# Kernel optimization log

Measured on AMD Instinct MI355X. Metric: run time of the kernel, lower is better.

Reference implementation:

```python
import jax, jax.numpy as jnp
import numpy as np

EPS = 1e-5

def _conv(x, w, b):
    # NCHW x OIHW -> NCHW, stride 1, SAME padding (stencil center (1,1) of 3x3, or 1x1)
    y = jax.lax.conv_general_dilated(x, w, (1, 1), 'SAME',
                                     dimension_numbers=('NCHW', 'OIHW', 'NCHW'))
    return y + b[None, :, None, None]

def _bn(x, gamma, beta):
    # training-mode batchnorm: stats over (N, H, W) per channel
    mean = jnp.mean(x, axis=(0, 2, 3), keepdims=True)
    var = jnp.var(x, axis=(0, 2, 3), keepdims=True)
    xhat = (x - mean) * jax.lax.rsqrt(var + EPS)
    return xhat * gamma[None, :, None, None] + beta[None, :, None, None]

def setup_inputs() -> dict:
    key = jax.random.key(0)
    ks = jax.random.split(key, 12)
    B, Cin, Cout, H, W = 2, 64, 64, 512, 512
    s = 0.05
    return {
        'x':  jax.random.normal(ks[0], (B, Cin, H, W), jnp.float32),
        'w1': jax.random.normal(ks[1], (Cout, Cin, 3, 3), jnp.float32) * s,
        'b1': jnp.zeros((Cout,), jnp.float32),
        'g1': jnp.ones((Cout,), jnp.float32),
        'be1': jnp.zeros((Cout,), jnp.float32),
        'w2': jax.random.normal(ks[2], (Cout, Cout, 3, 3), jnp.float32) * s,
        'b2': jnp.zeros((Cout,), jnp.float32),
        'g2': jnp.ones((Cout,), jnp.float32),
        'be2': jnp.zeros((Cout,), jnp.float32),
        'wp': jax.random.normal(ks[3], (Cout, Cin, 1, 1), jnp.float32) * s,
        'bp': jnp.zeros((Cout,), jnp.float32),
        'gp': jnp.ones((Cout,), jnp.float32),
        'bep': jnp.zeros((Cout,), jnp.float32),
    }

def reference(x, w1, b1, g1, be1, w2, b2, g2, be2, wp, bp, gp, bep):
    # project branch: 1x1 conv ([(0,0)] stencil) + BN
    residual = _bn(_conv(x, wp, bp), gp, bep)
    # conv1: pad + 3x3 lattice conv (full cp stencil) + BN + Identity downsample + ReLU
    out = jax.nn.relu(_bn(_conv(x, w1, b1), g1, be1))
    # conv2: pad + 3x3 lattice conv + BN
    out = _bn(_conv(out, w2, b2), g2, be2)
    # residual add + output ReLU
    return jax.nn.relu(out + residual)
```

## Files before the change

kernel.cpp:

```cpp
#include <hip/hip_runtime.h>
#include <hip/hip_bf16.h>
#include <stdint.h>

typedef short short8 __attribute__((ext_vector_type(8)));
typedef float f32x4 __attribute__((ext_vector_type(4)));
typedef float f32x16 __attribute__((ext_vector_type(16)));
typedef unsigned int u32;
typedef unsigned short u16;

#define HH 512
#define WW 512
#define CC 64
#define PLANE (HH*WW)
#define NSTATF 524288.0f

#define KTW 32
#define HSTR1 560
#define KBSTR1 1120
#define SLOTB1 4480
#define RING1 (8*SLOTB1)
#define HSTR2 592
#define KBSTR2 1184
#define SLOTB2 4736
#define NSLOT2 10
#define RING2 (NSLOT2*SLOTB2)
#define BOUNCEB 16384
#define NBC1 1024
#define NBC2 2048
#define K5S 132

__device__ __forceinline__ u16 f2bf(float f) {
  __hip_bfloat16 h = __float2bfloat16(f);
  return __builtin_bit_cast(u16, h);
}
__device__ __forceinline__ u32 pk2bf(float a, float b) {
  return (u32)f2bf(a) | ((u32)f2bf(b) << 16);
}
__device__ __forceinline__ float bf2f(u16 u) {
  u32 x = ((u32)u) << 16;
  return __builtin_bit_cast(float, x);
}
__device__ __forceinline__ void lds_barrier() {
  asm volatile("s_waitcnt lgkmcnt(0)" ::: "memory");
  __builtin_amdgcn_s_barrier();
  __builtin_amdgcn_sched_barrier(0);
}

__global__ __launch_bounds__(512) void kprep(const float* __restrict__ w1,
    const float* __restrict__ w2, const float* __restrict__ wp,
    u16* __restrict__ wb1, u16* __restrict__ wb2, u16* __restrict__ wbp)
{
  const int id = blockIdx.x*512 + threadIdx.x;
  const int lane = id & 63;
  if (id < 4608) {
    const int fid = id >> 6;
    const int ct4 = fid / 18, rem = fid % 18;
    const int tap = rem >> 1, kb = rem & 1;
    const int cout = ct4*16 + (lane & 15);
    const int k0c = kb*32 + (lane >> 4)*8;
    u32 ow[4];
#pragma unroll
    for (int p = 0; p < 4; ++p) {
      ow[p] = pk2bf(w1[(size_t)(cout*64 + k0c + p*2)*9 + tap],
                    w1[(size_t)(cout*64 + k0c + p*2 + 1)*9 + tap]);
    }
    *(uint4*)(wb1 + ((size_t)fid*64 + lane)*8) = make_uint4(ow[0],ow[1],ow[2],ow[3]);
  } else if (id < 9216) {
    const int fid = (id - 4608) >> 6;
    const int ct = fid / 36, rem = fid % 36;
    const int tap = rem >> 2, kb = rem & 3;
    const int cout = ct*32 + (lane & 31);
    const int cinb = kb*16 + (lane >> 5)*8;
    u32 ow[4];
#pragma unroll
    for (int p = 0; p < 4; ++p) {
      ow[p] = pk2bf(w2[(size_t)(cout*64 + cinb + p*2)*9 + tap],
                    w2[(size_t)(cout*64 + cinb + p*2 + 1)*9 + tap]);
    }
    *(uint4*)(wb2 + ((size_t)fid*64 + lane)*8) = make_uint4(ow[0],ow[1],ow[2],ow[3]);
  } else if (id < 9728) {
    const int fid = (id - 9216) >> 6;
    const int ct4 = fid >> 1, kb = fid & 1;
    const int cout = ct4*16 + (lane & 15);
    const int k0c = kb*32 + (lane >> 4)*8;
    u32 ow[4];
#pragma unroll
    for (int p = 0; p < 4; ++p)
      ow[p] = pk2bf(wp[cout*64 + k0c + p*2], wp[cout*64 + k0c + p*2 + 1]);
    *(uint4*)(wbp + ((size_t)fid*64 + lane)*8) = make_uint4(ow[0],ow[1],ow[2],ow[3]);
  }
}

__global__ __launch_bounds__(256) void k0(const float* __restrict__ x, u16* __restrict__ xh)
{
  __shared__ __align__(16) u32 Tp[32*260];
  const int tid = threadIdx.x;
  const int wt = blockIdx.x, h = blockIdx.y, n = blockIdx.z;
  const int w0 = wt*256;
  const float* xp = x + (size_t)n*CC*PLANE + (size_t)h*WW + w0;
#pragma unroll
  for (int it = 0; it < 8; ++it) {
    const int j = it*256 + tid;
    const int c2 = j >> 6, w4 = (j & 63) << 2;
    const f32x4 a = *(const f32x4*)(xp + (size_t)(c2*2    )*PLANE + w4);
    const f32x4 b = *(const f32x4*)(xp + (size_t)(c2*2 + 1)*PLANE + w4);
    uint4 o;
    o.x = pk2bf(a[0], b[0]);
    o.y = pk2bf(a[1], b[1]);
    o.z = pk2bf(a[2], b[2]);
    o.w = pk2bf(a[3], b[3]);
    *(uint4*)(Tp + (u32)c2*260 + (u32)(w4 ^ (4*(c2 >> 2)))) = o;
  }
  __syncthreads();
  u16* op = xh + ((size_t)(n*HH + h)*WW + w0)*CC;
#pragma unroll
  for (int it = 0; it < 8; ++it) {
    const int j = it*256 + tid;
    const int w = j >> 3, c8 = j & 7;
    const u32 wsw = (u32)(w ^ (4*c8));
    uint4 o;
    o.x = Tp[(u32)(c8*4 + 0)*260 + wsw];
    o.y = Tp[(u32)(c8*4 + 1)*260 + wsw];
    o.z = Tp[(u32)(c8*4 + 2)*260 + wsw];
    o.w = Tp[(u32)(c8*4 + 3)*260 + wsw];
    *(uint4*)(op + (size_t)w*CC + c8*8) = o;
  }
}

__global__ __launch_bounds__(256, 2) void kconv1(const u16* __restrict__ in,
    const u16* __restrict__ wb, const u16* __restrict__ wbp,
    u16* __restrict__ out, u16* __restrict__ yp,
    float* __restrict__ ps, float* __restrict__ pq,
    float* __restrict__ psp, float* __restrict__ pqp)
{
  __shared__ __align__(16) char LB[RING1 + BOUNCEB + 512];
  const int tid = threadIdx.x;
  const int lane = tid & 63, wv = tid >> 6;
  const int l15 = lane & 15, lq = lane >> 4;
  const int wt = blockIdx.x, hs = blockIdx.y, n = blockIdx.z;
  const int w0 = wt*KTW, h0 = hs*16;
  const int bid = (n*32 + hs)*16 + wt;

  short8 wfr[18];
#pragma unroll
  for (int f = 0; f < 18; ++f)
    wfr[f] = *(const short8*)(wb + ((size_t)(wv*18 + f)*64 + lane)*8);
  short8 wpf[2];
#pragma unroll
  for (int kb = 0; kb < 2; ++kb)
    wpf[kb] = *(const short8*)(wbp + ((size_t)(wv*2 + kb)*64 + lane)*8);

  float s4[4] = {0,0,0,0}, q4[4] = {0,0,0,0};
  float sp4[4] = {0,0,0,0}, qp4[4] = {0,0,0,0};
  const u16* inb = in + (size_t)n*PLANE*CC;
  const u32 co0 = (u32)((lq >> 1)*KBSTR1 + (lq & 1)*HSTR1);
  const u32 co1 = co0 + 2*KBSTR1;

  auto ld_one = [&](int j, int cl, int c8) -> uint4 {
    const int gh = h0 - 1 + j, gw = w0 - 1 + cl;
    if (((u32)gh < (u32)HH) && ((u32)gw < (u32)WW))
      return *(const uint4*)(inb + ((size_t)gh*WW + gw)*CC + c8*8);
    return make_uint4(0u,0u,0u,0u);
  };
  auto st_one = [&](int slot, int cl, int c8, uint4 v) {
    *(uint4*)(LB + (size_t)slot*SLOTB1 + (c8>>1)*KBSTR1 + (c8&1)*HSTR1 + cl*16) = v;
  };

  for (int idx = tid; idx < 4*272; idx += 256) {
    const int jj = idx / 272, rem = idx - jj*272;
    st_one(jj, rem >> 3, rem & 7, ld_one(jj, rem >> 3, rem & 7));
  }
  __syncthreads();

  uint4 st0, st1, st2;
  auto issue2 = [&](int jb) {
    { const int idx = tid;       const int jj = idx/272, rem = idx - jj*272;
      st0 = ld_one(jb + jj, rem >> 3, rem & 7); }
    { const int idx = 256 + tid; const int jj = idx/272, rem = idx - jj*272;
      st1 = ld_one(jb + jj, rem >> 3, rem & 7); }
    if (tid < 32) { const int idx = 512 + tid; const int jj = idx/272, rem = idx - jj*272;
      st2 = ld_one(jb + jj, rem >> 3, rem & 7); }
  };
  auto write2 = [&](int jb) {
    { const int idx = tid;       const int jj = idx/272, rem = idx - jj*272;
      st_one((jb + jj) & 7, rem >> 3, rem & 7, st0); }
    { const int idx = 256 + tid; const int jj = idx/272, rem = idx - jj*272;
      st_one((jb + jj) & 7, rem >> 3, rem & 7, st1); }
    if (tid < 32) { const int idx = 512 + tid; const int jj = idx/272, rem = idx - jj*272;
      st_one((jb + jj) & 7, rem >> 3, rem & 7, st2); }
  };

  issue2(4);

  for (int g = 0; g < 8; ++g) {
    if (g > 0) write2(2*g + 2);
    lds_barrier();
    if (g < 7) issue2(2*g + 4);

    const char* sb[4];
#pragma unroll
    for (int mi = 0; mi < 4; ++mi)
      sb[mi] = LB + (size_t)((2*g + mi) & 7)*SLOTB1 + l15*16;
    f32x4 a0t0, a0t1, a1t0, a1t1;
    f32x4 p0t0, p0t1, p1t0, p1t1;
#pragma unroll
    for (int r = 0; r < 4; ++r) {
      a0t0[r]=0.f; a0t1[r]=0.f; a1t0[r]=0.f; a1t1[r]=0.f;
      p0t0[r]=0.f; p0t1[r]=0.f; p1t0[r]=0.f; p1t1[r]=0.f;
    }
#pragma unroll
    for (int t = 0; t < 2; ++t) {
      const int pb = t*16;
#pragma unroll
      for (int kb = 0; kb < 2; ++kb) {
        const u32 ck = kb ? co1 : co0;
#pragma unroll
        for (int mi = 0; mi < 4; ++mi) {
#pragma unroll
          for (int kw = 0; kw < 3; ++kw) {
            const short8 X = *(const short8*)(sb[mi] + ck + (u32)((pb + kw)*16));
            if (mi <= 2) {
              const short8 Wf = wfr[(mi*3 + kw)*2 + kb];
              if (t == 0) a0t0 = __builtin_amdgcn_mfma_f32_16x16x32_bf16(Wf, X, a0t0, 0,0,0);
              else        a0t1 = __builtin_amdgcn_mfma_f32_16x16x32_bf16(Wf, X, a0t1, 0,0,0);
            }
            if (mi >= 1) {
              const short8 Wf = wfr[((mi-1)*3 + kw)*2 + kb];
              if (t == 0) a1t0 = __builtin_amdgcn_mfma_f32_16x16x32_bf16(Wf, X, a1t0, 0,0,0);
              else        a1t1 = __builtin_amdgcn_mfma_f32_16x16x32_bf16(Wf, X, a1t1, 0,0,0);
            }
            if (kw == 1 && mi == 1) {
              if (t == 0) p0t0 = __builtin_amdgcn_mfma_f32_16x16x32_bf16(wpf[kb], X, p0t0, 0,0,0);
              else        p0t1 = __builtin_amdgcn_mfma_f32_16x16x32_bf16(wpf[kb], X, p0t1, 0,0,0);
            }
            if (kw == 1 && mi == 2) {
              if (t == 0) p1t0 = __builtin_amdgcn_mfma_f32_16x16x32_bf16(wpf[kb], X, p1t0, 0,0,0);
              else        p1t1 = __builtin_amdgcn_mfma_f32_16x16x32_bf16(wpf[kb], X, p1t1, 0,0,0);
            }
          }
        }
      }
    }
    {
      const int co = wv*16 + lq*4;
#pragma unroll
      for (int r = 0; r < 4; ++r) {
        s4[r] += a0t0[r] + a0t1[r] + a1t0[r] + a1t1[r];
        q4[r] = fmaf(a0t0[r], a0t0[r], q4[r]);
        q4[r] = fmaf(a0t1[r], a0t1[r], q4[r]);
        q4[r] = fmaf(a1t0[r], a1t0[r], q4[r]);
        q4[r] = fmaf(a1t1[r], a1t1[r], q4[r]);
        sp4[r] += p0t0[r] + p0t1[r] + p1t0[r] + p1t1[r];
        qp4[r] = fmaf(p0t0[r], p0t0[r], qp4[r]);
        qp4[r] = fmaf(p0t1[r], p0t1[r], qp4[r]);
        qp4[r] = fmaf(p1t0[r], p1t0[r], qp4[r]);
        qp4[r] = fmaf(p1t1[r], p1t1[r], qp4[r]);
      }
#pragma unroll
      for (int t = 0; t < 2; ++t) {
        const int pos = t*16 + l15;
        const u32 addr = ((u32)(pos*128 + co*2)) ^ (((u32)(pos & 7)) << 4);
        uint2 c0, c1, d0, d1;
        if (t == 0) {
          c0.x = pk2bf(a0t0[0], a0t0[1]); c0.y = pk2bf(a0t0[2], a0t0[3]);
          c1.x = pk2bf(a1t0[0], a1t0[1]); c1.y = pk2bf(a1t0[2], a1t0[3]);
          d0.x = pk2bf(p0t0[0], p0t0[1]); d0.y = pk2bf(p0t0[2], p0t0[3]);
          d1.x = pk2bf(p1t0[0], p1t0[1]); d1.y = pk2bf(p1t0[2], p1t0[3]);
        } else {
          c0.x = pk2bf(a0t1[0], a0t1[1]); c0.y = pk2bf(a0t1[2], a0t1[3]);
          c1.x = pk2bf(a1t1[0], a1t1[1]); c1.y = pk2bf(a1t1[2], a1t1[3]);
          d0.x = pk2bf(p0t1[0], p0t1[1]); d0.y = pk2bf(p0t1[2], p0t1[3]);
          d1.x = pk2bf(p1t1[0], p1t1[1]); d1.y = pk2bf(p1t1[2], p1t1[3]);
        }
        *(uint2*)(LB + RING1 + 0*4096 + addr) = c0;
        *(uint2*)(LB + RING1 + 1*4096 + addr) = c1;
        *(uint2*)(LB + RING1 + 2*4096 + addr) = d0;
        *(uint2*)(LB + RING1 + 3*4096 + addr) = d1;
      }
    }
    lds_barrier();
    {
      const int rowi = tid >> 6, tt = tid & 63;
      const int pos = tt >> 1, half = (tt & 1)*64;
      const char* bb = LB + RING1 + rowi*4096;
      u16* base = (rowi < 2) ? out : yp;
      const int orow = h0 + 2*g + (rowi & 1);
      char* dst = (char*)base + ((size_t)((n*HH + orow)*WW + w0 + pos))*128 + half;
      const u32 sw = ((u32)(pos & 7)) << 4;
#pragma unroll
      for (int k2 = 0; k2 < 4; ++k2) {
        const uint4 v = *(const uint4*)(bb + (((u32)(pos*128 + half + k2*16)) ^ sw));
        *(uint4*)(dst + k2*16) = v;
      }
    }
  }

#pragma unroll
  for (int d = 1; d <= 8; d <<= 1) {
#pragma unroll
    for (int r = 0; r < 4; ++r) {
      s4[r] += __shfl_xor(s4[r], d, 64);
      q4[r] += __shfl_xor(q4[r], d, 64);
      sp4[r] += __shfl_xor(sp4[r], d, 64);
      qp4[r] += __shfl_xor(qp4[r], d, 64);
    }
  }
  if (l15 == 0) {
#pragma unroll
    for (int r = 0; r < 4; ++r) {
      const int co = wv*16 + lq*4 + r;
      ps[(size_t)co*NBC1 + bid] = s4[r];
      pq[(size_t)co*NBC1 + bid] = q4[r];
      psp[(size_t)co*NBC1 + bid] = sp4[r];
      pqp[(size_t)co*NBC1 + bid] = qp4[r];
    }
  }
}

__global__ __launch_bounds__(256, 2) void kconv2(const u16* __restrict__ in,
    const u16* __restrict__ wb,
    const float* __restrict__ As, const float* __restrict__ Bs,
    u16* __restrict__ out, float* __restrict__ ps, float* __restrict__ pq)
{
  __shared__ __align__(16) char LB[RING2 + BOUNCEB + 512];
  float* sA = (float*)(LB + RING2 + BOUNCEB);
  float* sB = sA + 64;
  const int tid = threadIdx.x;
  const int lane = tid & 63, wv = tid >> 6;
  const int ct = wv & 1, ro = wv >> 1;
  const int wt = blockIdx.x, hs = blockIdx.y, n = blockIdx.z;
  const int w0 = wt*KTW, h0 = hs*16;
  const int bid = (n*32 + hs)*16 + wt;

  if (tid < 64) { sA[tid] = As[tid]; sB[tid] = Bs[tid]; }
  __syncthreads();

  short8 wfr[36];
#pragma unroll
  for (int f = 0; f < 36; ++f)
    wfr[f] = *(const short8*)(wb + ((size_t)(ct*36 + f)*64 + lane)*8);
  float s[16], q[16];
#pragma unroll
  for (int r = 0; r < 16; ++r) { s[r] = 0.f; q[r] = 0.f; }

  const u16* inb = in + (size_t)n*PLANE*CC;
  const u32 lt = (u32)((lane & 31)*16 + (lane >> 5)*HSTR2);

  auto ld_one = [&](int j, int cl, int c8) -> uint4 {
    const int gh = h0 - 1 + j, gw = w0 - 1 + cl;
    if (((u32)gh < (u32)HH) && ((u32)gw < (u32)WW))
      return *(const uint4*)(inb + ((size_t)gh*WW + gw)*CC + c8*8);
    return make_uint4(0u,0u,0u,0u);
  };
  auto st_one = [&](int slot, int cl, int c8, uint4 v) {
    const u32* uw = (const u32*)&v;
    u32 ow[4];
    const int cb = c8*8;
#pragma unroll
    for (int h2 = 0; h2 < 4; ++h2) {
      float f0 = fmaxf(bf2f((u16)(uw[h2] & 0xFFFFu)) * sA[cb+h2*2]   + sB[cb+h2*2],   0.f);
      float f1 = fmaxf(bf2f((u16)(uw[h2] >> 16))     * sA[cb+h2*2+1] + sB[cb+h2*2+1], 0.f);
      ow[h2] = pk2bf(f0, f1);
    }
    *(uint4*)(LB + (size_t)slot*SLOTB2 + (c8>>1)*KBSTR2 + (c8&1)*HSTR2 + cl*16) =
        make_uint4(ow[0],ow[1],ow[2],ow[3]);
  };

  for (int idx = tid; idx < 6*272; idx += 256) {
    const int jj = idx / 272, rem = idx - jj*272;
    st_one(jj, rem >> 3, rem & 7, ld_one(jj, rem >> 3, rem & 7));
  }
  __syncthreads();

  for (int g = 0; g < 4; ++g) {
    const bool dostage = (g <= 2);
    const int jb = 4*g + 6;
    uint4 st0, st1, st2, st3, st4;
    if (dostage) {
      { const int idx = tid;        const int jj = idx/272, rem = idx - jj*272;
        st0 = ld_one(jb + jj, rem >> 3, rem & 7); }
      { const int idx = 256 + tid;  const int jj = idx/272, rem = idx - jj*272;
        st1 = ld_one(jb + jj, rem >> 3, rem & 7); }
      { const int idx = 512 + tid;  const int jj = idx/272, rem = idx - jj*272;
        st2 = ld_one(jb + jj, rem >> 3, rem & 7); }
      { const int idx = 768 + tid;  const int jj = idx/272, rem = idx - jj*272;
        st3 = ld_one(jb + jj, rem >> 3, rem & 7); }
      if (tid < 64) { const int idx = 1024 + tid; const int jj = idx/272, rem = idx - jj*272;
        st4 = ld_one(jb + jj, rem >> 3, rem & 7); }
    }

    const int r0 = 4*g + 2*ro;
    f32x16 acc0, acc1;
#pragma unroll
    for (int rr = 0; rr < 16; ++rr) { acc0[rr] = 0.f; acc1[rr] = 0.f; }
    {
      const char* bm[4];
#pragma unroll
      for (int mi = 0; mi < 4; ++mi) {
        int sl = r0 + mi; if (sl >= NSLOT2) sl -= NSLOT2;
        bm[mi] = LB + (size_t)sl*SLOTB2 + lt;
      }
#pragma unroll
      for (int kb = 0; kb < 4; ++kb) {
#pragma unroll
        for (int mi = 0; mi < 4; ++mi) {
          const char* bp_ = bm[mi] + kb*KBSTR2;
#pragma unroll
          for (int kw = 0; kw < 3; ++kw) {
            const short8 X = *(const short8*)(bp_ + kw*16);
            if (mi <= 2)
              acc0 = __builtin_amdgcn_mfma_f32_32x32x16_bf16(wfr[(mi*3+kw)*4+kb], X, acc0, 0,0,0);
            if (mi >= 1)
              acc1 = __builtin_amdgcn_mfma_f32_32x32x16_bf16(wfr[((mi-1)*3+kw)*4+kb], X, acc1, 0,0,0);
          }
        }
      }
    }
    {
      const int pos = lane & 31;
      const int cob = ct*32 + 4*(lane>>5);
#pragma unroll
      for (int rr = 0; rr < 16; ++rr) {
        const float v0 = acc0[rr], v1 = acc1[rr];
        s[rr] += v0 + v1;
        q[rr] = fmaf(v0, v0, q[rr]);
        q[rr] = fmaf(v1, v1, q[rr]);
      }
#pragma unroll
      for (int k = 0; k < 4; ++k) {
        const u32 addr = ((u32)(pos*128 + (cob + 8*k)*2)) ^ (((u32)(pos & 7)) << 4);
        uint2 p0, p1;
        p0.x = pk2bf(acc0[4*k],   acc0[4*k+1]);
        p0.y = pk2bf(acc0[4*k+2], acc0[4*k+3]);
        p1.x = pk2bf(acc1[4*k],   acc1[4*k+1]);
        p1.y = pk2bf(acc1[4*k+2], acc1[4*k+3]);
        *(uint2*)(LB + RING2 + (2*ro    )*4096 + addr) = p0;
        *(uint2*)(LB + RING2 + (2*ro + 1)*4096 + addr) = p1;
      }
    }
    lds_barrier();
    {
      const int rowi = tid >> 6, tt = tid & 63;
      const int pos = tt >> 1, half = (tt & 1)*64;
      const char* bb = LB + RING2 + rowi*4096;
      char* dst = (char*)out + ((size_t)((n*HH + h0 + 4*g + rowi)*WW + w0 + pos))*128 + half;
      const u32 sw = ((u32)(pos & 7)) << 4;
#pragma unroll
      for (int k2 = 0; k2 < 4; ++k2) {
        const uint4 v = *(const uint4*)(bb + (((u32)(pos*128 + half + k2*16)) ^ sw));
        *(uint4*)(dst + k2*16) = v;
      }
    }
    if (dostage) {
      { const int idx = tid;        const int jj = idx/272, rem = idx - jj*272;
        int sl = jb + jj; if (sl >= NSLOT2) sl -= NSLOT2;
        st_one(sl, rem >> 3, rem & 7, st0); }
      { const int idx = 256 + tid;  const int jj = idx/272, rem = idx - jj*272;
        int sl = jb + jj; if (sl >= NSLOT2) sl -= NSLOT2;
        st_one(sl, rem >> 3, rem & 7, st1); }
      { const int idx = 512 + tid;  const int jj = idx/272, rem = idx - jj*272;
        int sl = jb + jj; if (sl >= NSLOT2) sl -= NSLOT2;
        st_one(sl, rem >> 3, rem & 7, st2); }
      { const int idx = 768 + tid;  const int jj = idx/272, rem = idx - jj*272;
        int sl = jb + jj; if (sl >= NSLOT2) sl -= NSLOT2;
        st_one(sl, rem >> 3, rem & 7, st3); }
      if (tid < 64) { const int idx = 1024 + tid; const int jj = idx/272, rem = idx - jj*272;
        int sl = jb + jj; if (sl >= NSLOT2) sl -= NSLOT2;
        st_one(sl, rem >> 3, rem & 7, st4); }
    }
    lds_barrier();
  }

#pragma unroll
  for (int d = 1; d <= 16; d <<= 1) {
#pragma unroll
    for (int rr = 0; rr < 16; ++rr) {
      s[rr] += __shfl_xor(s[rr], d, 64);
      q[rr] += __shfl_xor(q[rr], d, 64);
    }
  }
  if ((lane & 31) == 0) {
#pragma unroll
    for (int rr = 0; rr < 16; ++rr) {
      const int co = ct*32 + (rr&3) + 8*(rr>>2) + 4*(lane>>5);
      ps[(size_t)co*NBC2 + bid*2 + ro] = s[rr];
      pq[(size_t)co*NBC2 + bid*2 + ro] = q[rr];
    }
  }
}

__global__ __launch_bounds__(256) void kfin2(
    const float* __restrict__ psA, const float* __restrict__ pqA,
    const float* __restrict__ gA, const float* __restrict__ beA,
    float* __restrict__ AA, float* __restrict__ BA, int cntA,
    const float* __restrict__ psB, const float* __restrict__ pqB,
    const float* __restrict__ gB, const float* __restrict__ beB,
    float* __restrict__ AB, float* __restrict__ BB, int cntB)
{
  const int blk = blockIdx.x;
  const bool second = blk >= 64;
  const int c = blk & 63;
  const float* psx = second ? psB : psA;
  const float* pqx = second ? pqB : pqA;
  const float* g  = second ? gB  : gA;
  const float* be = second ? beB : beA;
  float* A  = second ? AB : AA;
  float* Bc = second ? BB : BA;
  const int cnt = second ? cntB : cntA;

  const int t = threadIdx.x;
  float sv = 0.f, s2 = 0.f;
  const float* pr = psx + (size_t)c*cnt;
  const float* qr = pqx + (size_t)c*cnt;
  for (int k = t; k < cnt; k += 256) { sv += pr[k]; s2 += qr[k]; }
#pragma unroll
  for (int d = 1; d < 64; d <<= 1) { sv += __shfl_xor(sv, d, 64); s2 += __shfl_xor(s2, d, 64); }
  __shared__ float as_[4], aq_[4];
  if ((t & 63) == 0) { as_[t >> 6] = sv; aq_[t >> 6] = s2; }
  __syncthreads();
  if (t == 0) {
    sv = as_[0] + as_[1] + as_[2] + as_[3];
    s2 = aq_[0] + aq_[1] + aq_[2] + aq_[3];
    const float mean = sv / NSTATF;
    const float var = s2 / NSTATF - mean*mean;
    const float istd = rsqrtf(var + 1e-5f);
    const float a = g[c] * istd;
    A[c] = a;
    Bc[c] = be[c] - mean * a;
  }
}

__global__ __launch_bounds__(256) void k5(const u16* __restrict__ y2, const u16* __restrict__ yp,
    const float* __restrict__ A2, const float* __restrict__ B2c,
    const float* __restrict__ Ap, const float* __restrict__ Bp,
    float* __restrict__ outp)
{
  __shared__ float T[CC*K5S];
  __shared__ float cA2[64], cB2[64], cAp[64], cBp[64];
  const int tid = threadIdx.x;
  const int lane = tid & 63, wv = tid >> 6;
  const int wt = blockIdx.x, h = blockIdx.y, n = blockIdx.z;
  const int w0 = wt*128;
  if (tid < 64) { cA2[tid] = A2[tid]; cB2[tid] = B2c[tid]; cAp[tid] = Ap[tid]; cBp[tid] = Bp[tid]; }
  __syncthreads();
  const u16* p2 = y2 + ((size_t)(n*HH + h)*WW + w0)*CC;
  const u16* pp = yp + ((size_t)(n*HH + h)*WW + w0)*CC;
#pragma unroll
  for (int it = 0; it < 4; ++it) {
    const int j = it*256 + tid;
    const int w = j >> 3, c8 = j & 7;
    const uint4 u2 = *(const uint4*)(p2 + (size_t)w*CC + c8*8);
    const uint4 up = *(const uint4*)(pp + (size_t)w*CC + c8*8);
    const u32* m2 = (const u32*)&u2;
    const u32* mp = (const u32*)&up;
    const u32 sw = ((u32)(c8 & 3)) << 3;
#pragma unroll
    for (int h2 = 0; h2 < 4; ++h2) {
      const int c = c8*8 + h2*2;
      const float a = bf2f((u16)(m2[h2] & 0xFFFFu)), b = bf2f((u16)(m2[h2] >> 16));
      const float ra = bf2f((u16)(mp[h2] & 0xFFFFu)), rb = bf2f((u16)(mp[h2] >> 16));
      const u32 wsw = (u32)w ^ sw;
      T[(u32)(c    )*K5S + wsw] = fmaxf(a*cA2[c]   + cB2[c]   + ra*cAp[c]   + cBp[c],   0.f);
      T[(u32)(c + 1)*K5S + wsw] = fmaxf(b*cA2[c+1] + cB2[c+1] + rb*cAp[c+1] + cBp[c+1], 0.f);
    }
  }
  __syncthreads();
#pragma unroll
  for (int cc = 0; cc < 16; ++cc) {
    const int c = cc*4 + wv;
    const u32 sw = ((u32)((c >> 3) & 3)) << 3;
    const u32 idx = (u32)c*K5S + (((u32)(lane*2)) ^ sw);
    float2 v;
    v.x = T[idx];
    v.y = T[idx + 1];
    *(float2*)(outp + ((size_t)((n*CC + c)*HH + h))*WW + w0 + lane*2) = v;
  }
}

extern "C" void kernel_launch(void* const* d_in, const int* in_sizes, int n_in,
                              void* d_out, int out_size, void* d_ws, size_t ws_size,
                              hipStream_t stream)
{
  (void)in_sizes; (void)n_in; (void)out_size;
  const float* x   = (const float*)d_in[0];
  const float* w1  = (const float*)d_in[1];
  const float* g1  = (const float*)d_in[3];
  const float* be1 = (const float*)d_in[4];
  const float* w2  = (const float*)d_in[5];
  const float* g2  = (const float*)d_in[7];
  const float* be2 = (const float*)d_in[8];
  const float* wp  = (const float*)d_in[9];
  const float* gp  = (const float*)d_in[11];
  const float* bep = (const float*)d_in[12];

  const size_t TENB = (size_t)2*CC*PLANE*2;
  char* ws = (char*)d_ws;
  u16* bufA = (u16*)ws;
  u16* bufB = (u16*)(ws + TENB);
  u16* bufC = (u16*)(ws + TENB*2);
  char* aux = ws + TENB*3;
  u16* wb1 = (u16*)aux;
  u16* wb2 = (u16*)(aux + 73728);
  u16* wbp = (u16*)(aux + 147456);
  float* ps1 = (float*)(aux + 155648);
  float* pq1 = ps1 + 64*NBC1;
  float* psp = pq1 + 64*NBC1;
  float* pqp = psp + 64*NBC1;
  float* ps2 = pqp + 64*NBC1;
  float* pq2 = ps2 + 64*NBC2;
  float* A1  = pq2 + 64*NBC2;
  float* B1  = A1 + 64;
  float* A2  = B1 + 64;
  float* B2c = A2 + 64;
  float* Ap  = B2c + 64;
  float* Bp  = Ap + 64;
  const size_t need = (size_t)(Bp + 64 - (float*)ws) * 4;
  if (ws_size < need) return;

  kprep<<<19, 512, 0, stream>>>(w1, w2, wp, wb1, wb2, wbp);
  k0<<<dim3(2, HH, 2), 256, 0, stream>>>(x, bufA);
  kconv1<<<dim3(16, 32, 2), 256, 0, stream>>>(bufA, wb1, wbp,
                                              bufB, bufC, ps1, pq1, psp, pqp);
  kfin2<<<128, 256, 0, stream>>>(ps1, pq1, g1, be1, A1, B1, NBC1,
                                 psp, pqp, gp, bep, Ap, Bp, NBC1);
  kconv2<<<dim3(16, 32, 2), 256, 0, stream>>>(bufB, wb2, A1, B1,
                                              bufA, ps2, pq2);
  kfin2<<<64, 256, 0, stream>>>(ps2, pq2, g2, be2, A2, B2c, NBC2,
                                ps2, pq2, g2, be2, A2, B2c, NBC2);
  k5<<<dim3(4, HH, 2), 256, 0, stream>>>(bufA, bufC, A2, B2c, Ap, Bp, (float*)d_out);
}
```

Before: 249.1 us.

## Restructure conv2 to 16x16x32 MFMA with per-wave channel split and 8-slot ring

Conv2 now splits output channels across waves (16 per wave) using 16x16x32 bf16 MFMAs instead of 32x32x16 with a channel/row split. It also processes two output rows per iteration with an 8-slot LDS ring shared in layout with conv1. Global loads for the next rows are issued right after the barrier and written to LDS at the start of the following iteration. The aim is to cut register pressure (18 weight fragments instead of 36, smaller accumulators), shrink LDS, and overlap loads with compute. The cost is more iterations and barriers and smaller MFMA tiles with less operand reuse. The weight prep and stats partial-sum layout are unified with conv1's to match.

```diff
diff --git a/kernel.cpp b/kernel.cpp
--- a/kernel.cpp
+++ b/kernel.cpp
@@ -4,7 +4,6 @@
 
 typedef short short8 __attribute__((ext_vector_type(8)));
 typedef float f32x4 __attribute__((ext_vector_type(4)));
-typedef float f32x16 __attribute__((ext_vector_type(16)));
 typedef unsigned int u32;
 typedef unsigned short u16;
 
@@ -19,14 +18,9 @@
 #define KBSTR1 1120
 #define SLOTB1 4480
 #define RING1 (8*SLOTB1)
-#define HSTR2 592
-#define KBSTR2 1184
-#define SLOTB2 4736
-#define NSLOT2 10
-#define RING2 (NSLOT2*SLOTB2)
-#define BOUNCEB 16384
+#define BOUNCE1 16384
+#define BOUNCE2 8192
 #define NBC1 1024
-#define NBC2 2048
 #define K5S 132
 
 __device__ __forceinline__ u16 f2bf(float f) {
@@ -52,8 +46,10 @@
 {
   const int id = blockIdx.x*512 + threadIdx.x;
   const int lane = id & 63;
-  if (id < 4608) {
-    const int fid = id >> 6;
+  if (id < 9216) {
+    const float* w = (id < 4608) ? w1 : w2;
+    u16* o = (id < 4608) ? wb1 : wb2;
+    const int fid = (id < 4608) ? (id >> 6) : ((id - 4608) >> 6);
     const int ct4 = fid / 18, rem = fid % 18;
     const int tap = rem >> 1, kb = rem & 1;
     const int cout = ct4*16 + (lane & 15);
@@ -61,23 +57,10 @@
     u32 ow[4];
 #pragma unroll
     for (int p = 0; p < 4; ++p) {
-      ow[p] = pk2bf(w1[(size_t)(cout*64 + k0c + p*2)*9 + tap],
-                    w1[(size_t)(cout*64 + k0c + p*2 + 1)*9 + tap]);
-    }
-    *(uint4*)(wb1 + ((size_t)fid*64 + lane)*8) = make_uint4(ow[0],ow[1],ow[2],ow[3]);
-  } else if (id < 9216) {
-    const int fid = (id - 4608) >> 6;
-    const int ct = fid / 36, rem = fid % 36;
-    const int tap = rem >> 2, kb = rem & 3;
-    const int cout = ct*32 + (lane & 31);
-    const int cinb = kb*16 + (lane >> 5)*8;
-    u32 ow[4];
-#pragma unroll
-    for (int p = 0; p < 4; ++p) {
-      ow[p] = pk2bf(w2[(size_t)(cout*64 + cinb + p*2)*9 + tap],
-                    w2[(size_t)(cout*64 + cinb + p*2 + 1)*9 + tap]);
-    }
-    *(uint4*)(wb2 + ((size_t)fid*64 + lane)*8) = make_uint4(ow[0],ow[1],ow[2],ow[3]);
+      ow[p] = pk2bf(w[(size_t)(cout*64 + k0c + p*2)*9 + tap],
+                    w[(size_t)(cout*64 + k0c + p*2 + 1)*9 + tap]);
+    }
+    *(uint4*)(o + ((size_t)fid*64 + lane)*8) = make_uint4(ow[0],ow[1],ow[2],ow[3]);
   } else if (id < 9728) {
     const int fid = (id - 9216) >> 6;
     const int ct4 = fid >> 1, kb = fid & 1;
@@ -133,7 +116,7 @@
     float* __restrict__ ps, float* __restrict__ pq,
     float* __restrict__ psp, float* __restrict__ pqp)
 {
-  __shared__ __align__(16) char LB[RING1 + BOUNCEB + 512];
+  __shared__ __align__(16) char LB[RING1 + BOUNCE1 + 512];
   const int tid = threadIdx.x;
   const int lane = tid & 63, wv = tid >> 6;
   const int l15 = lane & 15, lq = lane >> 4;
@@ -322,12 +305,12 @@
     const float* __restrict__ As, const float* __restrict__ Bs,
     u16* __restrict__ out, float* __restrict__ ps, float* __restrict__ pq)
 {
-  __shared__ __align__(16) char LB[RING2 + BOUNCEB + 512];
-  float* sA = (float*)(LB + RING2 + BOUNCEB);
+  __shared__ __align__(16) char LB[RING1 + BOUNCE2 + 512];
+  float* sA = (float*)(LB + RING1 + BOUNCE2);
   float* sB = sA + 64;
   const int tid = threadIdx.x;
   const int lane = tid & 63, wv = tid >> 6;
-  const int ct = wv & 1, ro = wv >> 1;
+  const int l15 = lane & 15, lq = lane >> 4;
   const int wt = blockIdx.x, hs = blockIdx.y, n = blockIdx.z;
   const int w0 = wt*KTW, h0 = hs*16;
   const int bid = (n*32 + hs)*16 + wt;
@@ -335,16 +318,15 @@
   if (tid < 64) { sA[tid] = As[tid]; sB[tid] = Bs[tid]; }
   __syncthreads();
 
-  short8 wfr[36];
-#pragma unroll
-  for (int f = 0; f < 36; ++f)
-    wfr[f] = *(const short8*)(wb + ((size_t)(ct*36 + f)*64 + lane)*8);
-  float s[16], q[16];
-#pragma unroll
-  for (int r = 0; r < 16; ++r) { s[r] = 0.f; q[r] = 0.f; }
-
+  short8 wfr[18];
+#pragma unroll
+  for (int f = 0; f < 18; ++f)
+    wfr[f] = *(const short8*)(wb + ((size_t)(wv*18 + f)*64 + lane)*8);
+
+  float s4[4] = {0,0,0,0}, q4[4] = {0,0,0,0};
   const u16* inb = in + (size_t)n*PLANE*CC;
-  const u32 lt = (u32)((lane & 31)*16 + (lane >> 5)*HSTR2);
+  const u32 co0 = (u32)((lq >> 1)*KBSTR1 + (lq & 1)*HSTR1);
+  const u32 co1 = co0 + 2*KBSTR1;
 
   auto ld_one = [&](int j, int cl, int c8) -> uint4 {
     const int gh = h0 - 1 + j, gw = w0 - 1 + cl;
@@ -362,129 +344,127 @@
       float f1 = fmaxf(bf2f((u16)(uw[h2] >> 16))     * sA[cb+h2*2+1] + sB[cb+h2*2+1], 0.f);
       ow[h2] = pk2bf(f0, f1);
     }
-    *(uint4*)(LB + (size_t)slot*SLOTB2 + (c8>>1)*KBSTR2 + (c8&1)*HSTR2 + cl*16) =
+    *(uint4*)(LB + (size_t)slot*SLOTB1 + (c8>>1)*KBSTR1 + (c8&1)*HSTR1 + cl*16) =
         make_uint4(ow[0],ow[1],ow[2],ow[3]);
   };
 
-  for (int idx = tid; idx < 6*272; idx += 256) {
+  for (int idx = tid; idx < 4*272; idx += 256) {
     const int jj = idx / 272, rem = idx - jj*272;
     st_one(jj, rem >> 3, rem & 7, ld_one(jj, rem >> 3, rem & 7));
   }
   __syncthreads();
 
-  for (int g = 0; g < 4; ++g) {
-    const bool dostage = (g <= 2);
-    const int jb = 4*g + 6;
-    uint4 st0, st1, st2, st3, st4;
-    if (dostage) {
-      { const int idx = tid;        const int jj = idx/272, rem = idx - jj*272;
-        st0 = ld_one(jb + jj, rem >> 3, rem & 7); }
-      { const int idx = 256 + tid;  const int jj = idx/272, rem = idx - jj*272;
-        st1 = ld_one(jb + jj, rem >> 3, rem & 7); }
-      { const int idx = 512 + tid;  const int jj = idx/272, rem = idx - jj*272;
-        st2 = ld_one(jb + jj, rem >> 3, rem & 7); }
-      { const int idx = 768 + tid;  const int jj = idx/272, rem = idx - jj*272;
-        st3 = ld_one(jb + jj, rem >> 3, rem & 7); }
-      if (tid < 64) { const int idx = 1024 + tid; const int jj = idx/272, rem = idx - jj*272;
-        st4 = ld_one(jb + jj, rem >> 3, rem & 7); }
-    }
-
-    const int r0 = 4*g + 2*ro;
-    f32x16 acc0, acc1;
-#pragma unroll
-    for (int rr = 0; rr < 16; ++rr) { acc0[rr] = 0.f; acc1[rr] = 0.f; }
-    {
-      const char* bm[4];
-#pragma unroll
-      for (int mi = 0; mi < 4; ++mi) {
-        int sl = r0 + mi; if (sl >= NSLOT2) sl -= NSLOT2;
-        bm[mi] = LB + (size_t)sl*SLOTB2 + lt;
-      }
-#pragma unroll
-      for (int kb = 0; kb < 4; ++kb) {
+  uint4 st0, st1, st2;
+  auto issue2 = [&](int jb) {
+    { const int idx = tid;       const int jj = idx/272, rem = idx - jj*272;
+      st0 = ld_one(jb + jj, rem >> 3, rem & 7); }
+    { const int idx = 256 + tid; const int jj = idx/272, rem = idx - jj*272;
+      st1 = ld_one(jb + jj, rem >> 3, rem & 7); }
+    if (tid < 32) { const int idx = 512 + tid; const int jj = idx/272, rem = idx - jj*272;
+      st2 = ld_one(jb + jj, rem >> 3, rem & 7); }
+  };
+  auto write2 = [&](int jb) {
+    { const int idx = tid;       const int jj = idx/272, rem = idx - jj*272;
+      st_one((jb + jj) & 7, rem >> 3, rem & 7, st0); }
+    { const int idx = 256 + tid; const int jj = idx/272, rem = idx - jj*272;
+      st_one((jb + jj) & 7, rem >> 3, rem & 7, st1); }
+    if (tid < 32) { const int idx = 512 + tid; const int jj = idx/272, rem = idx - jj*272;
+      st_one((jb + jj) & 7, rem >> 3, rem & 7, st2); }
+  };
+
+  issue2(4);
+
+  for (int g = 0; g < 8; ++g) {
+    if (g > 0) write2(2*g + 2);
+    lds_barrier();
+    if (g < 7) issue2(2*g + 4);
+
+    const char* sb[4];
+#pragma unroll
+    for (int mi = 0; mi < 4; ++mi)
+      sb[mi] = LB + (size_t)((2*g + mi) & 7)*SLOTB1 + l15*16;
+    f32x4 a0t0, a0t1, a1t0, a1t1;
+#pragma unroll
+    for (int r = 0; r < 4; ++r) { a0t0[r]=0.f; a0t1[r]=0.f; a1t0[r]=0.f; a1t1[r]=0.f; }
+#pragma unroll
+    for (int t = 0; t < 2; ++t) {
+      const int pb = t*16;
+#pragma unroll
+      for (int kb = 0; kb < 2; ++kb) {
+        const u32 ck = kb ? co1 : co0;
 #pragma unroll
         for (int mi = 0; mi < 4; ++mi) {
-          const char* bp_ = bm[mi] + kb*KBSTR2;
 #pragma unroll
           for (int kw = 0; kw < 3; ++kw) {
-            const short8 X = *(const short8*)(bp_ + kw*16);
-            if (mi <= 2)
-              acc0 = __builtin_amdgcn_mfma_f32_32x32x16_bf16(wfr[(mi*3+kw)*4+kb], X, acc0, 0,0,0);
-            if (mi >= 1)
-              acc1 = __builtin_amdgcn_mfma_f32_32x32x16_bf16(wfr[((mi-1)*3+kw)*4+kb], X, acc1, 0,0,0);
+            const short8 X = *(const short8*)(sb[mi] + ck + (u32)((pb + kw)*16));
+            if (mi <= 2) {
+              const short8 Wf = wfr[(mi*3 + kw)*2 + kb];
+              if (t == 0) a0t0 = __builtin_amdgcn_mfma_f32_16x16x32_bf16(Wf, X, a0t0, 0,0,0);
+              else        a0t1 = __builtin_amdgcn_mfma_f32_16x16x32_bf16(Wf, X, a0t1, 0,0,0);
+            }
+            if (mi >= 1) {
+              const short8 Wf = wfr[((mi-1)*3 + kw)*2 + kb];
+              if (t == 0) a1t0 = __builtin_amdgcn_mfma_f32_16x16x32_bf16(Wf, X, a1t0, 0,0,0);
+              else        a1t1 = __builtin_amdgcn_mfma_f32_16x16x32_bf16(Wf, X, a1t1, 0,0,0);
+            }
           }
         }
       }
     }
     {
-      const int pos = lane & 31;
-      const int cob = ct*32 + 4*(lane>>5);
-#pragma unroll
-      for (int rr = 0; rr < 16; ++rr) {
-        const float v0 = acc0[rr], v1 = acc1[rr];
-        s[rr] += v0 + v1;
-        q[rr] = fmaf(v0, v0, q[rr]);
-        q[rr] = fmaf(v1, v1, q[rr]);
+      const int co = wv*16 + lq*4;
+#pragma unroll
+      for (int r = 0; r < 4; ++r) {
+        s4[r] += a0t0[r] + a0t1[r] + a1t0[r] + a1t1[r];
+        q4[r] = fmaf(a0t0[r], a0t0[r], q4[r]);
+        q4[r] = fmaf(a0t1[r], a0t1[r], q4[r]);
+        q4[r] = fmaf(a1t0[r], a1t0[r], q4[r]);
+        q4[r] = fmaf(a1t1[r], a1t1[r], q4[r]);
       }
 #pragma unroll
-      for (int k = 0; k < 4; ++k) {
-        const u32 addr = ((u32)(pos*128 + (cob + 8*k)*2)) ^ (((u32)(pos & 7)) << 4);
-        uint2 p0, p1;
-        p0.x = pk2bf(acc0[4*k],   acc0[4*k+1]);
-        p0.y = pk2bf(acc0[4*k+2], acc0[4*k+3]);
-        p1.x = pk2bf(acc1[4*k],   acc1[4*k+1]);
-        p1.y = pk2bf(acc1[4*k+2], acc1[4*k+3]);
-        *(uint2*)(LB + RING2 + (2*ro    )*4096 + addr) = p0;
-        *(uint2*)(LB + RING2 + (2*ro + 1)*4096 + addr) = p1;
+      for (int t = 0; t < 2; ++t) {
+        const int pos = t*16 + l15;
+        const u32 addr = ((u32)(pos*128 + co*2)) ^ (((u32)(pos & 7)) << 4);
+        uint2 c0, c1;
+        if (t == 0) {
+          c0.x = pk2bf(a0t0[0], a0t0[1]); c0.y = pk2bf(a0t0[2], a0t0[3]);
+          c1.x = pk2bf(a1t0[0], a1t0[1]); c1.y = pk2bf(a1t0[2], a1t0[3]);
+        } else {
+          c0.x = pk2bf(a0t1[0], a0t1[1]); c0.y = pk2bf(a0t1[2], a0t1[3]);
+          c1.x = pk2bf(a1t1[0], a1t1[1]); c1.y = pk2bf(a1t1[2], a1t1[3]);
+        }
+        *(uint2*)(LB + RING1 + 0*4096 + addr) = c0;
+        *(uint2*)(LB + RING1 + 1*4096 + addr) = c1;
       }
     }
     lds_barrier();
     {
-      const int rowi = tid >> 6, tt = tid & 63;
-      const int pos = tt >> 1, half = (tt & 1)*64;
-      const char* bb = LB + RING2 + rowi*4096;
-      char* dst = (char*)out + ((size_t)((n*HH + h0 + 4*g + rowi)*WW + w0 + pos))*128 + half;
-      const u32 sw = ((u32)(pos & 7)) << 4;
-#pragma unroll
-      for (int k2 = 0; k2 < 4; ++k2) {
-        const uint4 v = *(const uint4*)(bb + (((u32)(pos*128 + half + k2*16)) ^ sw));
-        *(uint4*)(dst + k2*16) = v;
-      }
-    }
-    if (dostage) {
-      { const int idx = tid;        const int jj = idx/272, rem = idx - jj*272;
-        int sl = jb + jj; if (sl >= NSLOT2) sl -= NSLOT2;
-        st_one(sl, rem >> 3, rem & 7, st0); }
-      { const int idx = 256 + tid;  const int jj = idx/272, rem = idx - jj*272;
-        int sl = jb + jj; if (sl >= NSLOT2) sl -= NSLOT2;
-        st_one(sl, rem >> 3, rem & 7, st1); }
-      { const int idx = 512 + tid;  const int jj = idx/272, rem = idx - jj*272;
-        int sl = jb + jj; if (sl >= NSLOT2) sl -= NSLOT2;
-        st_one(sl, rem >> 3, rem & 7, st2); }
-      { const int idx = 768 + tid;  const int jj = idx/272, rem = idx - jj*272;
-        int sl = jb + jj; if (sl >= NSLOT2) sl -= NSLOT2;
-        st_one(sl, rem >> 3, rem & 7, st3); }
-      if (tid < 64) { const int idx = 1024 + tid; const int jj = idx/272, rem = idx - jj*272;
-        int sl = jb + jj; if (sl >= NSLOT2) sl -= NSLOT2;
-        st_one(sl, rem >> 3, rem & 7, st4); }
-    }
-    lds_barrier();
-  }
-
-#pragma unroll
-  for (int d = 1; d <= 16; d <<= 1) {
-#pragma unroll
-    for (int rr = 0; rr < 16; ++rr) {
-      s[rr] += __shfl_xor(s[rr], d, 64);
-      q[rr] += __shfl_xor(q[rr], d, 64);
-    }
-  }
-  if ((lane & 31) == 0) {
-#pragma unroll
-    for (int rr = 0; rr < 16; ++rr) {
-      const int co = ct*32 + (rr&3) + 8*(rr>>2) + 4*(lane>>5);
-      ps[(size_t)co*NBC2 + bid*2 + ro] = s[rr];
-      pq[(size_t)co*NBC2 + bid*2 + ro] = q[rr];
+      const int rowi = tid >> 7, tt = tid & 127;
+      const int pos = tt >> 2, qb = (tt & 3)*32;
+      const char* bb = LB + RING1 + rowi*4096;
+      const u32 a0 = ((u32)(pos*128 + qb)) ^ (((u32)(pos & 7)) << 4);
+      const uint4 v0 = *(const uint4*)(bb + a0);
+      const uint4 v1 = *(const uint4*)(bb + (a0 ^ 16u));
+      char* dst = (char*)out + ((size_t)((n*HH + h0 + 2*g + rowi)*WW + w0 + pos))*128 + qb;
+      *(uint4*)dst = v0;
+      *(uint4*)(dst + 16) = v1;
+    }
+  }
+
+#pragma unroll
+  for (int d = 1; d <= 8; d <<= 1) {
+#pragma unroll
+    for (int r = 0; r < 4; ++r) {
+      s4[r] += __shfl_xor(s4[r], d, 64);
+      q4[r] += __shfl_xor(q4[r], d, 64);
+    }
+  }
+  if (l15 == 0) {
+#pragma unroll
+    for (int r = 0; r < 4; ++r) {
+      const int co = wv*16 + lq*4 + r;
+      ps[(size_t)co*NBC1 + bid] = s4[r];
+      pq[(size_t)co*NBC1 + bid] = q4[r];
     }
   }
 }
@@ -607,8 +587,8 @@
   float* psp = pq1 + 64*NBC1;
   float* pqp = psp + 64*NBC1;
   float* ps2 = pqp + 64*NBC1;
-  float* pq2 = ps2 + 64*NBC2;
-  float* A1  = pq2 + 64*NBC2;
+  float* pq2 = ps2 + 64*NBC1;
+  float* A1  = pq2 + 64*NBC1;
   float* B1  = A1 + 64;
   float* A2  = B1 + 64;
   float* B2c = A2 + 64;
@@ -625,7 +605,7 @@
                                  psp, pqp, gp, bep, Ap, Bp, NBC1);
   kconv2<<<dim3(16, 32, 2), 256, 0, stream>>>(bufB, wb2, A1, B1,
                                               bufA, ps2, pq2);
-  kfin2<<<64, 256, 0, stream>>>(ps2, pq2, g2, be2, A2, B2c, NBC2,
-                                ps2, pq2, g2, be2, A2, B2c, NBC2);
+  kfin2<<<64, 256, 0, stream>>>(ps2, pq2, g2, be2, A2, B2c, NBC1,
+                                ps2, pq2, g2, be2, A2, B2c, NBC1);
   k5<<<dim3(4, HH, 2), 256, 0, stream>>>(bufA, bufC, A2, B2c, Ap, Bp, (float*)d_out);
 }
```

Result: faster. 215.4 us (-13.5%).
